# Performance work log

Measured on AMD Instinct MI355X. Metric: run time of the kernel, lower is better.

Reference implementation:

```python
import jax, jax.numpy as jnp
import numpy as np

B, N, C = 8, 16384, 40
E, KD, VD = 512, 256, 256


def setup_inputs() -> dict:
    key = jax.random.key(0)
    ks = jax.random.split(key, 10)
    s = 0.02
    return {
        "q": jax.random.normal(ks[0], (B, N, E), jnp.float32),
        "k": jax.random.normal(ks[1], (B, C, KD), jnp.float32),
        "v": jax.random.normal(ks[2], (B, C, VD), jnp.float32),
        "coarse_pred": jax.random.normal(ks[3], (B, C, N), jnp.float32),
        "Wq": jax.random.normal(ks[4], (E, E), jnp.float32) * s,
        "bq": jnp.zeros((E,), jnp.float32),
        "Wk": jax.random.normal(ks[5], (E, KD), jnp.float32) * s,
        "bk": jnp.zeros((E,), jnp.float32),
        "Wv": jax.random.normal(ks[6], (E, VD), jnp.float32) * s,
        "bv": jnp.zeros((E,), jnp.float32),
    }


def reference(q, k, v, coarse_pred, Wq, bq, Wk, bk, Wv, bv):
    # Projections (nn.Linear: x @ W.T + b)
    qp = jnp.einsum("bne,fe->bnf", q, Wq) + bq          # (B, N, E)
    kp = jnp.einsum("bcd,fd->bcf", k, Wk) + bk          # (B, C, E)
    vp = jnp.einsum("bcd,fd->bcf", v, Wv) + bv          # (B, C, E)

    scale = 1.0 / jnp.sqrt(jnp.float32(E))
    attn = jnp.einsum("bne,bce->bnc", qp, kp) * scale   # (B, N, C)
    attn = jax.nn.softmax(attn, axis=-1)

    # coarse_pred is detached, transposed to (B, N, C), softmaxed over classes
    cp = jax.nn.softmax(jnp.swapaxes(coarse_pred, 1, 2), axis=-1)
    attn = jax.nn.softmax(attn * cp, axis=-1)

    out = jnp.einsum("bnc,bce->bne", attn, vp)          # (B, N, E)
    return out
```

## Files before the change

### kernel.cpp

```cpp
#include <hip/hip_runtime.h>
#include <stdint.h>

#define Bb 8
#define Nn 16384
#define Cc 40
#define Ee 512
#define Dd 256

typedef __attribute__((ext_vector_type(4))) float f32x4;
typedef __attribute__((ext_vector_type(8))) short bf16x8;

__device__ __forceinline__ unsigned short f2bf(float f) {
  union { float f; uint32_t u; } x; x.f = f;
  uint32_t r = x.u + 0x7FFFu + ((x.u >> 16) & 1u);
  return (unsigned short)(r >> 16);
}
__device__ __forceinline__ unsigned int pack2(float a, float b) {
  return (unsigned int)f2bf(a) | ((unsigned int)f2bf(b) << 16);
}

__global__ __launch_bounds__(256) void prepA_kernel(
    const float* __restrict__ Wq, const float* __restrict__ Wk,
    const float* __restrict__ bq, const float* __restrict__ bk,
    float* __restrict__ Mt, float* __restrict__ tvec,
    float* __restrict__ uvec, float* __restrict__ bqbk) {
  const int t = threadIdx.x;
  if (blockIdx.x == 8) {
    if (blockIdx.z != 0) return;
    const int by = blockIdx.y;
    if (by < 2) {
      const int e = by * 256 + t;
      float s = 0.f;
      #pragma unroll 8
      for (int f = 0; f < Ee; f++) s += Wq[(size_t)f * Ee + e] * bk[f];
      tvec[e] = s;
    } else if (by == 2) {
      const int d = t;
      float s = 0.f;
      #pragma unroll 8
      for (int f = 0; f < Ee; f++) s += Wk[(size_t)f * Dd + d] * bq[f];
      uvec[d] = s;
    } else {
      __shared__ float red[256];
      float p = 0.f;
      for (int f = t; f < Ee; f += 256) p += bq[f] * bk[f];
      red[t] = p; __syncthreads();
      #pragma unroll
      for (int off = 128; off > 0; off >>= 1) {
        if (t < off) red[t] += red[t + off];
        __syncthreads();
      }
      if (t == 0) bqbk[0] = red[0];
    }
    return;
  }
  __shared__ float WqL[64][68];
  __shared__ float WkL[64][68];
  const int te = (t & 15) * 4;
  const int td = (t >> 4) * 4;
  const int ebase = blockIdx.x * 64, dbase = blockIdx.y * 64;
  const int fbase = blockIdx.z * 256;
  f32x4 acc0 = {0,0,0,0}, acc1 = {0,0,0,0}, acc2 = {0,0,0,0}, acc3 = {0,0,0,0};
  for (int f0 = 0; f0 < 256; f0 += 64) {
    __syncthreads();
    #pragma unroll
    for (int i = 0; i < 4; i++) {
      int idx = t + i * 256;
      int row = idx >> 4, c4 = (idx & 15) * 4;
      *(float4*)&WqL[row][c4] = *(const float4*)(Wq + (size_t)(fbase + f0 + row) * Ee + ebase + c4);
      *(float4*)&WkL[row][c4] = *(const float4*)(Wk + (size_t)(fbase + f0 + row) * Dd + dbase + c4);
    }
    __syncthreads();
    #pragma unroll 8
    for (int ff = 0; ff < 64; ff++) {
      float4 a = *(const float4*)&WkL[ff][td];
      float4 b = *(const float4*)&WqL[ff][te];
      acc0[0] += a.x*b.x; acc0[1] += a.x*b.y; acc0[2] += a.x*b.z; acc0[3] += a.x*b.w;
      acc1[0] += a.y*b.x; acc1[1] += a.y*b.y; acc1[2] += a.y*b.z; acc1[3] += a.y*b.w;
      acc2[0] += a.z*b.x; acc2[1] += a.z*b.y; acc2[2] += a.z*b.z; acc2[3] += a.z*b.w;
      acc3[0] += a.w*b.x; acc3[1] += a.w*b.y; acc3[2] += a.w*b.z; acc3[3] += a.w*b.w;
    }
  }
  float* mt = Mt + (size_t)blockIdx.z * 131072;
  *(f32x4*)&mt[(size_t)(dbase + td + 0) * Ee + ebase + te] = acc0;
  *(f32x4*)&mt[(size_t)(dbase + td + 1) * Ee + ebase + te] = acc1;
  *(f32x4*)&mt[(size_t)(dbase + td + 2) * Ee + ebase + te] = acc2;
  *(f32x4*)&mt[(size_t)(dbase + td + 3) * Ee + ebase + te] = acc3;
}

__global__ __launch_bounds__(256) void prepB_kernel(
    const float* __restrict__ k, const float* __restrict__ v,
    const float* __restrict__ Wv, const float* __restrict__ bv,
    const float* __restrict__ Mt, const float* __restrict__ tvec,
    const float* __restrict__ uvec, const float* __restrict__ bqbk,
    unsigned short* __restrict__ abf, unsigned short* __restrict__ vpf,
    float* __restrict__ dbias) {
  __shared__ float xL[8][Dd];
  const int t = threadIdx.x;
  const int el = t & 127, half = t >> 7;
  const int e = blockIdx.y * 128 + el;

  if (blockIdx.x < 48) {
    const int sbase = blockIdx.x * 8;
    for (int i = t; i < 8 * Dd; i += 256) {
      int row = i >> 8, dd = i & (Dd - 1);
      int sg = sbase + row, bb_ = sg / 48, cc = sg % 48;
      xL[row][dd] = (cc < 40) ? k[((size_t)bb_ * Cc + cc) * Dd + dd] : 0.f;
    }
    __syncthreads();
    float acc[4] = {0,0,0,0};
    float db[4]  = {0,0,0,0};
    #pragma unroll 4
    for (int d = 0; d < Dd; d++) {
      float mt = Mt[(size_t)d * Ee + e] + Mt[131072 + (size_t)d * Ee + e];
      float ud = uvec[d];
      #pragma unroll
      for (int si = 0; si < 4; si++) {
        float kv = xL[half*4 + si][d];
        acc[si] += mt * kv;
        db[si]  += ud * kv;
      }
    }
    const float scale = 0.044194173824159216f;
    const float te = tvec[e];
    const float bqbkv = bqbk[0];
    const int ks = e >> 5, gg = (e >> 3) & 3, j = e & 7;
    #pragma unroll
    for (int si = 0; si < 4; si++) {
      int sg = sbase + half*4 + si, bb_ = sg / 48, cc = sg % 48;
      int ct = cc >> 4, lane16 = (cc & 15) + 16*gg;
      unsigned short val = (cc < 40) ? f2bf(scale * (acc[si] + te)) : (unsigned short)0;
      abf[((((size_t)bb_*3 + ct)*16 + ks)*64 + lane16)*8 + j] = val;
      if (el == 0) dbias[bb_*64 + cc] = (cc < 40) ? scale * (db[si] + bqbkv) : 0.f;
    }
  } else {
    const int sbase = (blockIdx.x - 48) * 8;
    for (int i = t; i < 8 * Dd; i += 256) {
      int row = i >> 8, dd = i & (Dd - 1);
      int sg = sbase + row, bb_ = sg >> 6, cc = sg & 63;
      xL[row][dd] = (cc < 40) ? v[((size_t)bb_ * Cc + cc) * Dd + dd] : 0.f;
    }
    __syncthreads();
    const float* wrow = Wv + (size_t)e * Dd;
    float acc[4] = {0,0,0,0};
    #pragma unroll 2
    for (int dd = 0; dd < Dd; dd += 4) {
      float4 w = *(const float4*)(wrow + dd);
      #pragma unroll
      for (int si = 0; si < 4; si++) {
        float4 vv = *(const float4*)&xL[half*4 + si][dd];
        acc[si] += w.x*vv.x + w.y*vv.y + w.z*vv.z + w.w*vv.w;
      }
    }
    const float bve = bv[e];
    const int nt = e >> 4, elan = e & 15;
    #pragma unroll
    for (int si = 0; si < 4; si++) {
      int sg = sbase + half*4 + si, bb_ = sg >> 6, cc = sg & 63;
      int s = cc >> 5, gg = (cc >> 3) & 3, j = cc & 7;
      unsigned short val = (cc < 40) ? f2bf(acc[si] + bve) : (unsigned short)0;
      vpf[((((size_t)bb_*32 + nt)*2 + s)*64 + (elan + 16*gg))*8 + j] = val;
    }
  }
}

__global__ __launch_bounds__(64, 4) void main_kernel(
    const float* __restrict__ q, const float* __restrict__ coarse,
    const unsigned short* __restrict__ abfrag,
    const unsigned short* __restrict__ vpfrag,
    const float* __restrict__ dbias, float* __restrict__ out) {
  __shared__ unsigned short s_att[16][72];
  const int lane = threadIdx.x;
  const int r = lane & 15, g = lane >> 4;
  const int bid = blockIdx.x;
  const int b = bid >> 10;
  const int nw = (bid & 1023) << 4;
  const float* qrow = q + ((size_t)b * Nn + nw + r) * Ee + 8 * g;
  const bf16x8* abf = (const bf16x8*)abfrag + (size_t)b * 3 * 16 * 64 + lane;
  const bool v2 = (g < 2);

  f32x4 acc0 = {0,0,0,0}, acc1 = {0,0,0,0}, acc2 = {0,0,0,0};
  float4 A0[8], A1[8];

  #pragma unroll
  for (int j = 0; j < 4; j++) {
    A0[2*j]   = *(const float4*)(qrow + 32*j);
    A0[2*j+1] = *(const float4*)(qrow + 32*j + 4);
  }
  #pragma unroll
  for (int j = 0; j < 4; j++) {
    A1[2*j]   = *(const float4*)(qrow + 128 + 32*j);
    A1[2*j+1] = *(const float4*)(qrow + 128 + 32*j + 4);
  }

  const float* cbase = coarse + (size_t)b * Cc * Nn + (nw + r);
  float cr[3][4];
  #pragma unroll
  for (int rg = 0; rg < 4; rg++) {
    cr[0][rg] = cbase[(size_t)( 0 + 4*g + rg) * Nn];
    cr[1][rg] = cbase[(size_t)(16 + 4*g + rg) * Nn];
    cr[2][rg] = v2 ? cbase[(size_t)(32 + 4*g + rg) * Nn] : -3e38f;
  }
  float4 db0 = *(const float4*)(dbias + b*64 +  0 + 4*g);
  float4 db1 = *(const float4*)(dbias + b*64 + 16 + 4*g);
  float4 db2 = *(const float4*)(dbias + b*64 + 32 + 4*g);

  auto COMP = [&](const float4* A, int c) {
    #pragma unroll
    for (int j = 0; j < 4; j++) {
      float4 qa = A[2*j], qc = A[2*j+1];
      bf16x8 qf;
      qf[0]=(short)f2bf(qa.x); qf[1]=(short)f2bf(qa.y);
      qf[2]=(short)f2bf(qa.z); qf[3]=(short)f2bf(qa.w);
      qf[4]=(short)f2bf(qc.x); qf[5]=(short)f2bf(qc.y);
      qf[6]=(short)f2bf(qc.z); qf[7]=(short)f2bf(qc.w);
      const int ks = 4*c + j;
      acc0 = __builtin_amdgcn_mfma_f32_16x16x32_bf16(abf[(0*16+ks)*64], qf, acc0, 0,0,0);
      acc1 = __builtin_amdgcn_mfma_f32_16x16x32_bf16(abf[(1*16+ks)*64], qf, acc1, 0,0,0);
      acc2 = __builtin_amdgcn_mfma_f32_16x16x32_bf16(abf[(2*16+ks)*64], qf, acc2, 0,0,0);
    }
  };

  COMP(A0, 0);
  #pragma unroll
  for (int j = 0; j < 4; j++) {
    A0[2*j]   = *(const float4*)(qrow + 256 + 32*j);
    A0[2*j+1] = *(const float4*)(qrow + 256 + 32*j + 4);
  }
  COMP(A1, 1);
  #pragma unroll
  for (int j = 0; j < 4; j++) {
    A1[2*j]   = *(const float4*)(qrow + 384 + 32*j);
    A1[2*j+1] = *(const float4*)(qrow + 384 + 32*j + 4);
  }
  COMP(A0, 2);
  COMP(A1, 3);

  float L[3][4];
  #pragma unroll
  for (int rg = 0; rg < 4; rg++) {
    L[0][rg] = acc0[rg] + ((const float*)&db0)[rg];
    L[1][rg] = acc1[rg] + ((const float*)&db1)[rg];
    L[2][rg] = acc2[rg] + ((const float*)&db2)[rg];
  }

  float m1 = -3e38f;
  #pragma unroll
  for (int rg = 0; rg < 4; rg++) {
    m1 = fmaxf(m1, L[0][rg]); m1 = fmaxf(m1, L[1][rg]);
    if (v2) m1 = fmaxf(m1, L[2][rg]);
  }
  m1 = fmaxf(m1, __shfl_xor(m1, 16));
  m1 = fmaxf(m1, __shfl_xor(m1, 32));
  float p[3][4]; float s1 = 0.f;
  #pragma unroll
  for (int rg = 0; rg < 4; rg++) {
    p[0][rg] = __expf(L[0][rg] - m1); s1 += p[0][rg];
    p[1][rg] = __expf(L[1][rg] - m1); s1 += p[1][rg];
    p[2][rg] = v2 ? __expf(L[2][rg] - m1) : 0.f; s1 += p[2][rg];
  }
  s1 += __shfl_xor(s1, 16); s1 += __shfl_xor(s1, 32);
  const float inv1 = 1.0f / s1;

  float m2 = -3e38f;
  #pragma unroll
  for (int rg = 0; rg < 4; rg++) {
    m2 = fmaxf(m2, cr[0][rg]); m2 = fmaxf(m2, cr[1][rg]);
    if (v2) m2 = fmaxf(m2, cr[2][rg]);
  }
  m2 = fmaxf(m2, __shfl_xor(m2, 16));
  m2 = fmaxf(m2, __shfl_xor(m2, 32));
  float cpv[3][4]; float s2 = 0.f;
  #pragma unroll
  for (int rg = 0; rg < 4; rg++) {
    cpv[0][rg] = __expf(cr[0][rg] - m2); s2 += cpv[0][rg];
    cpv[1][rg] = __expf(cr[1][rg] - m2); s2 += cpv[1][rg];
    cpv[2][rg] = v2 ? __expf(cr[2][rg] - m2) : 0.f; s2 += cpv[2][rg];
  }
  s2 += __shfl_xor(s2, 16); s2 += __shfl_xor(s2, 32);
  const float inv2 = 1.0f / s2;

  const float sc12 = inv1 * inv2;
  float w[3][4];
  float m3 = -3e38f;
  #pragma unroll
  for (int rg = 0; rg < 4; rg++) {
    w[0][rg] = p[0][rg] * cpv[0][rg] * sc12;
    w[1][rg] = p[1][rg] * cpv[1][rg] * sc12;
    w[2][rg] = v2 ? (p[2][rg] * cpv[2][rg] * sc12) : 0.f;
    m3 = fmaxf(m3, w[0][rg]); m3 = fmaxf(m3, w[1][rg]);
    if (v2) m3 = fmaxf(m3, w[2][rg]);
  }
  m3 = fmaxf(m3, __shfl_xor(m3, 16));
  m3 = fmaxf(m3, __shfl_xor(m3, 32));
  float p3[3][4]; float s3 = 0.f;
  #pragma unroll
  for (int rg = 0; rg < 4; rg++) {
    p3[0][rg] = __expf(w[0][rg] - m3); s3 += p3[0][rg];
    p3[1][rg] = __expf(w[1][rg] - m3); s3 += p3[1][rg];
    p3[2][rg] = v2 ? __expf(w[2][rg] - m3) : 0.f; s3 += p3[2][rg];
  }
  s3 += __shfl_xor(s3, 16); s3 += __shfl_xor(s3, 32);
  const float inv3 = 1.0f / s3;

  unsigned int* srow = (unsigned int*)&s_att[r][0];
  #pragma unroll
  for (int ct = 0; ct < 3; ct++) {
    srow[8*ct + 2*g + 0] = pack2(p3[ct][0]*inv3, p3[ct][1]*inv3);
    srow[8*ct + 2*g + 1] = pack2(p3[ct][2]*inv3, p3[ct][3]*inv3);
  }
  srow[24 + 2*g + 0] = 0u;
  srow[24 + 2*g + 1] = 0u;
  asm volatile("s_waitcnt lgkmcnt(0)" ::: "memory");
  const bf16x8 pa0 = *(const bf16x8*)&s_att[r][ 0 + 8*g];
  const bf16x8 pa1 = *(const bf16x8*)&s_att[r][32 + 8*g];

  const bf16x8* vpf = (const bf16x8*)vpfrag + (size_t)b * 32 * 2 * 64 + lane;
  float* outb = out + ((size_t)b * Nn + nw) * Ee;
  #pragma unroll 8
  for (int nt = 0; nt < 32; nt++) {
    bf16x8 vf0 = vpf[(nt*2 + 0)*64];
    bf16x8 vf1 = vpf[(nt*2 + 1)*64];
    f32x4 o = {0,0,0,0};
    o = __builtin_amdgcn_mfma_f32_16x16x32_bf16(pa0, vf0, o, 0,0,0);
    o = __builtin_amdgcn_mfma_f32_16x16x32_bf16(pa1, vf1, o, 0,0,0);
    #pragma unroll
    for (int rg = 0; rg < 4; rg++)
      outb[(size_t)(4*g + rg) * Ee + nt*16 + r] = o[rg];
  }
}

extern "C" void kernel_launch(void* const* d_in, const int* in_sizes, int n_in,
                              void* d_out, int out_size, void* d_ws, size_t ws_size,
                              hipStream_t stream) {
  const float* q   = (const float*)d_in[0];
  const float* k   = (const float*)d_in[1];
  const float* v   = (const float*)d_in[2];
  const float* cps = (const float*)d_in[3];
  const float* Wq  = (const float*)d_in[4];
  const float* bq  = (const float*)d_in[5];
  const float* Wk  = (const float*)d_in[6];
  const float* bk  = (const float*)d_in[7];
  const float* Wv  = (const float*)d_in[8];
  const float* bv  = (const float*)d_in[9];
  float* out = (float*)d_out;
  char* ws = (char*)d_ws;

  float*          Mt    = (float*)(ws);
  float*          tvec  = (float*)(ws + 1048576);
  float*          uvec  = (float*)(ws + 1050624);
  float*          bqbkp = (float*)(ws + 1051648);
  unsigned short* abf   = (unsigned short*)(ws + 1052672);
  unsigned short* vpf   = (unsigned short*)(ws + 1052672 + 393216);
  float*          dbias = (float*)(ws + 1052672 + 393216 + 524288);

  prepA_kernel<<<dim3(9, 4, 2), 256, 0, stream>>>(Wq, Wk, bq, bk, Mt, tvec, uvec, bqbkp);
  prepB_kernel<<<dim3(112, 4),  256, 0, stream>>>(k, v, Wv, bv, Mt, tvec, uvec, bqbkp,
                                                  abf, vpf, dbias);
  main_kernel <<<dim3(8192),     64, 0, stream>>>(q, cps, abf, vpf, dbias, out);
}
```

Baseline: 206.1 us.

## Stage per-batch fragments in LDS and make main kernel persistent over rows

Main kernel moves from 8192 single-wave blocks to 256 blocks of 8 waves. Each block loads the per-batch K-side and V-side bf16 fragments into shared memory once, and each wave loops over 4 row tiles while prefetching the next tile's q rows. The second MFMA swaps its operands so each lane writes a contiguous float4 of output, and q conversion uses the packed hardware bf16 intrinsic. The risks are fewer blocks than the grid had before, about 115KB of LDS and high register pressure limiting occupancy, and a small unroll change in prepB.

After: 174.6 us. 15.3% less time.

```diff
diff --git a/kernel.cpp b/kernel.cpp
--- a/kernel.cpp
+++ b/kernel.cpp
@@ -1,4 +1,5 @@
 #include <hip/hip_runtime.h>
+#include <hip/hip_bf16.h>
 #include <stdint.h>
 
 #define Bb 8
@@ -17,6 +18,14 @@
 }
 __device__ __forceinline__ unsigned int pack2(float a, float b) {
   return (unsigned int)f2bf(a) | ((unsigned int)f2bf(b) << 16);
+}
+__device__ __forceinline__ bf16x8 q2bf(float4 a, float4 c) {
+  union { __hip_bfloat162 h2[4]; bf16x8 v; } u;
+  u.h2[0] = __float22bfloat162_rn(float2{a.x, a.y});
+  u.h2[1] = __float22bfloat162_rn(float2{a.z, a.w});
+  u.h2[2] = __float22bfloat162_rn(float2{c.x, c.y});
+  u.h2[3] = __float22bfloat162_rn(float2{c.z, c.w});
+  return u.v;
 }
 
 __global__ __launch_bounds__(256) void prepA_kernel(
@@ -110,7 +119,7 @@
     __syncthreads();
     float acc[4] = {0,0,0,0};
     float db[4]  = {0,0,0,0};
-    #pragma unroll 4
+    #pragma unroll 8
     for (int d = 0; d < Dd; d++) {
       float mt = Mt[(size_t)d * Ee + e] + Mt[131072 + (size_t)d * Ee + e];
       float ud = uvec[d];
@@ -164,169 +173,170 @@
   }
 }
 
-__global__ __launch_bounds__(64, 4) void main_kernel(
+__global__ __launch_bounds__(512, 2) void main_kernel(
     const float* __restrict__ q, const float* __restrict__ coarse,
     const unsigned short* __restrict__ abfrag,
     const unsigned short* __restrict__ vpfrag,
     const float* __restrict__ dbias, float* __restrict__ out) {
-  __shared__ unsigned short s_att[16][72];
-  const int lane = threadIdx.x;
+  __shared__ uint4 fragL[7168];
+  __shared__ unsigned short s_att[8][16][72];
+  const int t = threadIdx.x;
+  const int wave = t >> 6, lane = t & 63;
   const int r = lane & 15, g = lane >> 4;
-  const int bid = blockIdx.x;
-  const int b = bid >> 10;
-  const int nw = (bid & 1023) << 4;
-  const float* qrow = q + ((size_t)b * Nn + nw + r) * Ee + 8 * g;
-  const bf16x8* abf = (const bf16x8*)abfrag + (size_t)b * 3 * 16 * 64 + lane;
+  const int b = blockIdx.x >> 5;
+  const int seg = blockIdx.x & 31;
   const bool v2 = (g < 2);
 
-  f32x4 acc0 = {0,0,0,0}, acc1 = {0,0,0,0}, acc2 = {0,0,0,0};
-  float4 A0[8], A1[8];
-
-  #pragma unroll
-  for (int j = 0; j < 4; j++) {
-    A0[2*j]   = *(const float4*)(qrow + 32*j);
-    A0[2*j+1] = *(const float4*)(qrow + 32*j + 4);
-  }
-  #pragma unroll
-  for (int j = 0; j < 4; j++) {
-    A1[2*j]   = *(const float4*)(qrow + 128 + 32*j);
-    A1[2*j+1] = *(const float4*)(qrow + 128 + 32*j + 4);
-  }
-
-  const float* cbase = coarse + (size_t)b * Cc * Nn + (nw + r);
-  float cr[3][4];
-  #pragma unroll
-  for (int rg = 0; rg < 4; rg++) {
-    cr[0][rg] = cbase[(size_t)( 0 + 4*g + rg) * Nn];
-    cr[1][rg] = cbase[(size_t)(16 + 4*g + rg) * Nn];
-    cr[2][rg] = v2 ? cbase[(size_t)(32 + 4*g + rg) * Nn] : -3e38f;
-  }
-  float4 db0 = *(const float4*)(dbias + b*64 +  0 + 4*g);
-  float4 db1 = *(const float4*)(dbias + b*64 + 16 + 4*g);
-  float4 db2 = *(const float4*)(dbias + b*64 + 32 + 4*g);
-
-  auto COMP = [&](const float4* A, int c) {
-    #pragma unroll
-    for (int j = 0; j < 4; j++) {
-      float4 qa = A[2*j], qc = A[2*j+1];
-      bf16x8 qf;
-      qf[0]=(short)f2bf(qa.x); qf[1]=(short)f2bf(qa.y);
-      qf[2]=(short)f2bf(qa.z); qf[3]=(short)f2bf(qa.w);
-      qf[4]=(short)f2bf(qc.x); qf[5]=(short)f2bf(qc.y);
-      qf[6]=(short)f2bf(qc.z); qf[7]=(short)f2bf(qc.w);
-      const int ks = 4*c + j;
-      acc0 = __builtin_amdgcn_mfma_f32_16x16x32_bf16(abf[(0*16+ks)*64], qf, acc0, 0,0,0);
-      acc1 = __builtin_amdgcn_mfma_f32_16x16x32_bf16(abf[(1*16+ks)*64], qf, acc1, 0,0,0);
-      acc2 = __builtin_amdgcn_mfma_f32_16x16x32_bf16(abf[(2*16+ks)*64], qf, acc2, 0,0,0);
+  const float4 db0 = *(const float4*)(dbias + b*64 +  0 + 4*g);
+  const float4 db1 = *(const float4*)(dbias + b*64 + 16 + 4*g);
+  const float4 db2 = *(const float4*)(dbias + b*64 + 32 + 4*g);
+
+  {
+    const uint4* srcA = (const uint4*)abfrag + (size_t)b * 3072;
+    #pragma unroll
+    for (int i = 0; i < 6; i++) fragL[t + i*512] = srcA[t + i*512];
+    const uint4* srcV = (const uint4*)vpfrag + (size_t)b * 4096;
+    #pragma unroll
+    for (int i = 0; i < 8; i++) fragL[3072 + t + i*512] = srcV[t + i*512];
+  }
+  __syncthreads();
+
+  const int row0 = seg * 512 + wave * 16;
+  const float* qrow0 = q + ((size_t)b * Nn + row0 + r) * Ee + 8 * g;
+  const float* cbase0 = coarse + (size_t)b * Cc * Nn + row0 + r;
+  float* outb0 = out + ((size_t)b * Nn + row0 + r) * Ee + 4 * g;
+
+  f32x4 acc0, acc1, acc2;
+  float4 H0[16], H1[16];
+
+  auto LOADH = [&](const float* qr, int h, float4* H) {
+    #pragma unroll
+    for (int j = 0; j < 8; j++) {
+      H[2*j]   = *(const float4*)(qr + 256*h + 32*j);
+      H[2*j+1] = *(const float4*)(qr + 256*h + 32*j + 4);
     }
   };
-
-  COMP(A0, 0);
-  #pragma unroll
-  for (int j = 0; j < 4; j++) {
-    A0[2*j]   = *(const float4*)(qrow + 256 + 32*j);
-    A0[2*j+1] = *(const float4*)(qrow + 256 + 32*j + 4);
-  }
-  COMP(A1, 1);
-  #pragma unroll
-  for (int j = 0; j < 4; j++) {
-    A1[2*j]   = *(const float4*)(qrow + 384 + 32*j);
-    A1[2*j+1] = *(const float4*)(qrow + 384 + 32*j + 4);
-  }
-  COMP(A0, 2);
-  COMP(A1, 3);
-
-  float L[3][4];
-  #pragma unroll
-  for (int rg = 0; rg < 4; rg++) {
-    L[0][rg] = acc0[rg] + ((const float*)&db0)[rg];
-    L[1][rg] = acc1[rg] + ((const float*)&db1)[rg];
-    L[2][rg] = acc2[rg] + ((const float*)&db2)[rg];
-  }
-
-  float m1 = -3e38f;
-  #pragma unroll
-  for (int rg = 0; rg < 4; rg++) {
-    m1 = fmaxf(m1, L[0][rg]); m1 = fmaxf(m1, L[1][rg]);
-    if (v2) m1 = fmaxf(m1, L[2][rg]);
-  }
-  m1 = fmaxf(m1, __shfl_xor(m1, 16));
-  m1 = fmaxf(m1, __shfl_xor(m1, 32));
-  float p[3][4]; float s1 = 0.f;
-  #pragma unroll
-  for (int rg = 0; rg < 4; rg++) {
-    p[0][rg] = __expf(L[0][rg] - m1); s1 += p[0][rg];
-    p[1][rg] = __expf(L[1][rg] - m1); s1 += p[1][rg];
-    p[2][rg] = v2 ? __expf(L[2][rg] - m1) : 0.f; s1 += p[2][rg];
-  }
-  s1 += __shfl_xor(s1, 16); s1 += __shfl_xor(s1, 32);
-  const float inv1 = 1.0f / s1;
-
-  float m2 = -3e38f;
-  #pragma unroll
-  for (int rg = 0; rg < 4; rg++) {
-    m2 = fmaxf(m2, cr[0][rg]); m2 = fmaxf(m2, cr[1][rg]);
-    if (v2) m2 = fmaxf(m2, cr[2][rg]);
-  }
-  m2 = fmaxf(m2, __shfl_xor(m2, 16));
-  m2 = fmaxf(m2, __shfl_xor(m2, 32));
-  float cpv[3][4]; float s2 = 0.f;
-  #pragma unroll
-  for (int rg = 0; rg < 4; rg++) {
-    cpv[0][rg] = __expf(cr[0][rg] - m2); s2 += cpv[0][rg];
-    cpv[1][rg] = __expf(cr[1][rg] - m2); s2 += cpv[1][rg];
-    cpv[2][rg] = v2 ? __expf(cr[2][rg] - m2) : 0.f; s2 += cpv[2][rg];
-  }
-  s2 += __shfl_xor(s2, 16); s2 += __shfl_xor(s2, 32);
-  const float inv2 = 1.0f / s2;
-
-  const float sc12 = inv1 * inv2;
-  float w[3][4];
-  float m3 = -3e38f;
-  #pragma unroll
-  for (int rg = 0; rg < 4; rg++) {
-    w[0][rg] = p[0][rg] * cpv[0][rg] * sc12;
-    w[1][rg] = p[1][rg] * cpv[1][rg] * sc12;
-    w[2][rg] = v2 ? (p[2][rg] * cpv[2][rg] * sc12) : 0.f;
-    m3 = fmaxf(m3, w[0][rg]); m3 = fmaxf(m3, w[1][rg]);
-    if (v2) m3 = fmaxf(m3, w[2][rg]);
-  }
-  m3 = fmaxf(m3, __shfl_xor(m3, 16));
-  m3 = fmaxf(m3, __shfl_xor(m3, 32));
-  float p3[3][4]; float s3 = 0.f;
-  #pragma unroll
-  for (int rg = 0; rg < 4; rg++) {
-    p3[0][rg] = __expf(w[0][rg] - m3); s3 += p3[0][rg];
-    p3[1][rg] = __expf(w[1][rg] - m3); s3 += p3[1][rg];
-    p3[2][rg] = v2 ? __expf(w[2][rg] - m3) : 0.f; s3 += p3[2][rg];
-  }
-  s3 += __shfl_xor(s3, 16); s3 += __shfl_xor(s3, 32);
-  const float inv3 = 1.0f / s3;
-
-  unsigned int* srow = (unsigned int*)&s_att[r][0];
-  #pragma unroll
-  for (int ct = 0; ct < 3; ct++) {
-    srow[8*ct + 2*g + 0] = pack2(p3[ct][0]*inv3, p3[ct][1]*inv3);
-    srow[8*ct + 2*g + 1] = pack2(p3[ct][2]*inv3, p3[ct][3]*inv3);
-  }
-  srow[24 + 2*g + 0] = 0u;
-  srow[24 + 2*g + 1] = 0u;
-  asm volatile("s_waitcnt lgkmcnt(0)" ::: "memory");
-  const bf16x8 pa0 = *(const bf16x8*)&s_att[r][ 0 + 8*g];
-  const bf16x8 pa1 = *(const bf16x8*)&s_att[r][32 + 8*g];
-
-  const bf16x8* vpf = (const bf16x8*)vpfrag + (size_t)b * 32 * 2 * 64 + lane;
-  float* outb = out + ((size_t)b * Nn + nw) * Ee;
-  #pragma unroll 8
-  for (int nt = 0; nt < 32; nt++) {
-    bf16x8 vf0 = vpf[(nt*2 + 0)*64];
-    bf16x8 vf1 = vpf[(nt*2 + 1)*64];
-    f32x4 o = {0,0,0,0};
-    o = __builtin_amdgcn_mfma_f32_16x16x32_bf16(pa0, vf0, o, 0,0,0);
-    o = __builtin_amdgcn_mfma_f32_16x16x32_bf16(pa1, vf1, o, 0,0,0);
-    #pragma unroll
-    for (int rg = 0; rg < 4; rg++)
-      outb[(size_t)(4*g + rg) * Ee + nt*16 + r] = o[rg];
+  auto COMP = [&](const float4* H, int h) {
+    #pragma unroll
+    for (int j = 0; j < 8; j++) {
+      bf16x8 qf = q2bf(H[2*j], H[2*j+1]);
+      const int ks = 8*h + j;
+      acc0 = __builtin_amdgcn_mfma_f32_16x16x32_bf16(*(const bf16x8*)&fragL[(0*16+ks)*64 + lane], qf, acc0, 0,0,0);
+      acc1 = __builtin_amdgcn_mfma_f32_16x16x32_bf16(*(const bf16x8*)&fragL[(1*16+ks)*64 + lane], qf, acc1, 0,0,0);
+      acc2 = __builtin_amdgcn_mfma_f32_16x16x32_bf16(*(const bf16x8*)&fragL[(2*16+ks)*64 + lane], qf, acc2, 0,0,0);
+    }
+  };
+
+  LOADH(qrow0, 0, H0);
+
+  for (int it = 0; it < 4; it++) {
+    const float* qr = qrow0 + (size_t)(it*128) * Ee;
+    LOADH(qr, 1, H1);
+    acc0 = f32x4{0,0,0,0}; acc1 = f32x4{0,0,0,0}; acc2 = f32x4{0,0,0,0};
+    COMP(H0, 0);
+
+    const float* cb = cbase0 + it*128;
+    float cr[3][4];
+    #pragma unroll
+    for (int rg = 0; rg < 4; rg++) {
+      cr[0][rg] = cb[(size_t)( 0 + 4*g + rg) * Nn];
+      cr[1][rg] = cb[(size_t)(16 + 4*g + rg) * Nn];
+      cr[2][rg] = v2 ? cb[(size_t)(32 + 4*g + rg) * Nn] : -3e38f;
+    }
+
+    COMP(H1, 1);
+
+    float L[3][4];
+    #pragma unroll
+    for (int rg = 0; rg < 4; rg++) {
+      L[0][rg] = acc0[rg] + ((const float*)&db0)[rg];
+      L[1][rg] = acc1[rg] + ((const float*)&db1)[rg];
+      L[2][rg] = acc2[rg] + ((const float*)&db2)[rg];
+    }
+
+    float m1 = -3e38f;
+    #pragma unroll
+    for (int rg = 0; rg < 4; rg++) {
+      m1 = fmaxf(m1, L[0][rg]); m1 = fmaxf(m1, L[1][rg]);
+      if (v2) m1 = fmaxf(m1, L[2][rg]);
+    }
+    m1 = fmaxf(m1, __shfl_xor(m1, 16));
+    m1 = fmaxf(m1, __shfl_xor(m1, 32));
+    float p[3][4]; float s1 = 0.f;
+    #pragma unroll
+    for (int rg = 0; rg < 4; rg++) {
+      p[0][rg] = __expf(L[0][rg] - m1); s1 += p[0][rg];
+      p[1][rg] = __expf(L[1][rg] - m1); s1 += p[1][rg];
+      p[2][rg] = v2 ? __expf(L[2][rg] - m1) : 0.f; s1 += p[2][rg];
+    }
+    s1 += __shfl_xor(s1, 16); s1 += __shfl_xor(s1, 32);
+    const float inv1 = 1.0f / s1;
+
+    float m2 = -3e38f;
+    #pragma unroll
+    for (int rg = 0; rg < 4; rg++) {
+      m2 = fmaxf(m2, cr[0][rg]); m2 = fmaxf(m2, cr[1][rg]);
+      if (v2) m2 = fmaxf(m2, cr[2][rg]);
+    }
+    m2 = fmaxf(m2, __shfl_xor(m2, 16));
+    m2 = fmaxf(m2, __shfl_xor(m2, 32));
+    float cpv[3][4]; float s2 = 0.f;
+    #pragma unroll
+    for (int rg = 0; rg < 4; rg++) {
+      cpv[0][rg] = __expf(cr[0][rg] - m2); s2 += cpv[0][rg];
+      cpv[1][rg] = __expf(cr[1][rg] - m2); s2 += cpv[1][rg];
+      cpv[2][rg] = v2 ? __expf(cr[2][rg] - m2) : 0.f; s2 += cpv[2][rg];
+    }
+    s2 += __shfl_xor(s2, 16); s2 += __shfl_xor(s2, 32);
+    const float inv2 = 1.0f / s2;
+
+    const float sc12 = inv1 * inv2;
+    float w[3][4];
+    float m3 = -3e38f;
+    #pragma unroll
+    for (int rg = 0; rg < 4; rg++) {
+      w[0][rg] = p[0][rg] * cpv[0][rg] * sc12;
+      w[1][rg] = p[1][rg] * cpv[1][rg] * sc12;
+      w[2][rg] = v2 ? (p[2][rg] * cpv[2][rg] * sc12) : 0.f;
+      m3 = fmaxf(m3, w[0][rg]); m3 = fmaxf(m3, w[1][rg]);
+      if (v2) m3 = fmaxf(m3, w[2][rg]);
+    }
+    m3 = fmaxf(m3, __shfl_xor(m3, 16));
+    m3 = fmaxf(m3, __shfl_xor(m3, 32));
+    float p3[3][4]; float s3 = 0.f;
+    #pragma unroll
+    for (int rg = 0; rg < 4; rg++) {
+      p3[0][rg] = __expf(w[0][rg] - m3); s3 += p3[0][rg];
+      p3[1][rg] = __expf(w[1][rg] - m3); s3 += p3[1][rg];
+      p3[2][rg] = v2 ? __expf(w[2][rg] - m3) : 0.f; s3 += p3[2][rg];
+    }
+    s3 += __shfl_xor(s3, 16); s3 += __shfl_xor(s3, 32);
+    const float inv3 = 1.0f / s3;
+
+    if (it < 3) LOADH(qrow0 + (size_t)((it+1)*128) * Ee, 0, H0);
+
+    unsigned int* srow = (unsigned int*)&s_att[wave][r][0];
+    #pragma unroll
+    for (int ct = 0; ct < 3; ct++) {
+      srow[8*ct + 2*g + 0] = pack2(p3[ct][0]*inv3, p3[ct][1]*inv3);
+      srow[8*ct + 2*g + 1] = pack2(p3[ct][2]*inv3, p3[ct][3]*inv3);
+    }
+    srow[24 + 2*g + 0] = 0u;
+    srow[24 + 2*g + 1] = 0u;
+    asm volatile("s_waitcnt lgkmcnt(0)" ::: "memory");
+    const bf16x8 pa0 = *(const bf16x8*)&s_att[wave][r][ 0 + 8*g];
+    const bf16x8 pa1 = *(const bf16x8*)&s_att[wave][r][32 + 8*g];
+
+    float* outp = outb0 + (size_t)(it*128) * Ee;
+    #pragma unroll 8
+    for (int nt = 0; nt < 32; nt++) {
+      bf16x8 vf0 = *(const bf16x8*)&fragL[3072 + (nt*2 + 0)*64 + lane];
+      bf16x8 vf1 = *(const bf16x8*)&fragL[3072 + (nt*2 + 1)*64 + lane];
+      f32x4 o = {0,0,0,0};
+      o = __builtin_amdgcn_mfma_f32_16x16x32_bf16(vf0, pa0, o, 0,0,0);
+      o = __builtin_amdgcn_mfma_f32_16x16x32_bf16(vf1, pa1, o, 0,0,0);
+      *(f32x4*)(outp + nt*16) = o;
+    }
   }
 }
 
@@ -357,5 +367,5 @@
   prepA_kernel<<<dim3(9, 4, 2), 256, 0, stream>>>(Wq, Wk, bq, bk, Mt, tvec, uvec, bqbkp);
   prepB_kernel<<<dim3(112, 4),  256, 0, stream>>>(k, v, Wv, bv, Mt, tvec, uvec, bqbkp,
                                                   abf, vpf, dbias);
-  main_kernel <<<dim3(8192),     64, 0, stream>>>(q, cps, abf, vpf, dbias, out);
-}
+  main_kernel <<<dim3(256),     512, 0, stream>>>(q, cps, abf, vpf, dbias, out);
+}
```
